# Performance work log

Hardware: AMD Instinct MI355X
Metric: run time of the kernel (lower is better)

## Reference

```python
import jax, jax.numpy as jnp
import numpy as np

N = 100000
E = 1600000
IN_C = 256
HID = 256
OUT_C = 10
G = 64  # number of graphs in batch


def setup_inputs() -> dict:
    key = jax.random.key(0)
    k1, k2, k3, k4, k5, k6, k7 = jax.random.split(key, 7)
    x = jax.random.normal(k1, (N, IN_C), dtype=jnp.float32)
    edge_index = jax.random.randint(k2, (2, E), 0, N, dtype=jnp.int64)
    batch = jnp.sort(jax.random.randint(k3, (N,), 0, G, dtype=jnp.int64))
    # GCNConv weight (glorot-ish) and bias
    W1 = jax.random.normal(k4, (IN_C, HID), dtype=jnp.float32) / np.sqrt(IN_C)
    b1 = jnp.zeros((HID,), dtype=jnp.float32)
    # final Linear
    W2 = jax.random.normal(k5, (HID, OUT_C), dtype=jnp.float32) / np.sqrt(HID)
    b2 = jax.random.normal(k6, (OUT_C,), dtype=jnp.float32) * 0.01
    return {"x": x, "edge_index": edge_index, "batch": batch,
            "W1": W1, "b1": b1, "W2": W2, "b2": b2}


def reference(x, edge_index, batch, W1, b1, W2, b2):
    # ---- GCNConv(in_channels, hidden_dim), add_self_loops=True, symmetric norm ----
    src = edge_index[0]
    dst = edge_index[1]
    loop = jnp.arange(N, dtype=src.dtype)
    src = jnp.concatenate([src, loop])  # [E+N]
    dst = jnp.concatenate([dst, loop])
    # degree on destination nodes (incl. self-loops) -> >= 1 everywhere
    deg = jax.ops.segment_sum(jnp.ones_like(dst, dtype=x.dtype), dst, num_segments=N)
    dinv = jax.lax.rsqrt(deg)  # deg >= 1, safe
    h = x @ W1  # linear transform first (PyG GCNConv order)
    norm = dinv[src] * dinv[dst]  # [E+N]
    msgs = h[src] * norm[:, None]  # gather + scale
    agg = jax.ops.segment_sum(msgs, dst, num_segments=N) + b1  # scatter-add + bias
    # ---- relu; dropout is identity in eval mode ----
    hrelu = jax.nn.relu(agg)
    # ---- global_mean_pool over batch ids ----
    sums = jax.ops.segment_sum(hrelu, batch, num_segments=G)
    counts = jax.ops.segment_sum(jnp.ones((N,), dtype=x.dtype), batch, num_segments=G)
    pooled = sums / jnp.maximum(counts, 1.0)[:, None]  # [G, HID]
    # ---- final linear ----
    return pooled @ W2 + b2
```

## Files before the change

kernel.cpp:

```cpp
#include <hip/hip_runtime.h>

#define NN 100000
#define EE 1600000
#define C 256
#define OUTC 10
#define NG 64

#define NBK 391
#define CHUNK 16384
#define NBLK1 ((EE + CHUNK - 1) / CHUNK)
#define PADSLACK 2048

#define NODES_PER_GROUP 8
#define NODES_PER_BLOCK 32

typedef __bf16 bf16x8 __attribute__((ext_vector_type(8)));
typedef float f32x4 __attribute__((ext_vector_type(4)));
typedef float f32x2 __attribute__((ext_vector_type(2)));

__device__ __forceinline__ ushort f2bf(float f) {
    unsigned u = __float_as_uint(f);
    return (ushort)((u + 0x7fffu + ((u >> 16) & 1u)) >> 16);
}
__device__ __forceinline__ bf16x8 as_bf16x8(uint4 v) {
    union { uint4 u; bf16x8 b; } c; c.u = v; return c.b;
}

__device__ __forceinline__ uchar f2fp8(float f) {
    return (uchar)(__builtin_amdgcn_cvt_pk_fp8_f32(f, 0.f, 0, false) & 0xff);
}
__device__ __forceinline__ void acc_fp8x4(float4& s, unsigned v) {
    f32x2 lo = __builtin_amdgcn_cvt_pk_f32_fp8(v, false);
    f32x2 hi = __builtin_amdgcn_cvt_pk_f32_fp8(v, true);
    s.x += lo[0]; s.y += lo[1]; s.z += hi[0]; s.w += hi[1];
}

__global__ __launch_bounds__(1024) void count_kernel(const int* __restrict__ batch,
                                                     float* __restrict__ cnt) {
    __shared__ int h[NG];
    if (threadIdx.x < NG) h[threadIdx.x] = 0;
    __syncthreads();
    int i = blockIdx.x * blockDim.x + threadIdx.x;
    if (i < NN) atomicAdd(&h[batch[i]], 1);
    __syncthreads();
    if (threadIdx.x < NG) {
        int v = h[threadIdx.x];
        if (v > 0) atomicAdd(&cnt[threadIdx.x], (float)v);
    }
}

__global__ __launch_bounds__(256) void bucket_hist_kernel(const int* __restrict__ ei,
                                                          int* __restrict__ bhist) {
    __shared__ int h[NBK];
    for (int t = threadIdx.x; t < NBK; t += 256) h[t] = 0;
    __syncthreads();
    const int base = blockIdx.x * CHUNK;
    const int end = min(base + CHUNK, EE);
    for (int e = base + threadIdx.x; e < end; e += 256)
        atomicAdd(&h[ei[EE + e] >> 8], 1);
    __syncthreads();
    for (int t = threadIdx.x; t < NBK; t += 256)
        if (h[t]) atomicAdd(&bhist[t], h[t]);
}

__global__ __launch_bounds__(512) void bucket_scan_kernel(const int* __restrict__ bhist,
                                                          int* __restrict__ bbase,
                                                          int* __restrict__ bcur) {
    __shared__ int sc[512];
    const int t = threadIdx.x;
    int v = (t < NBK) ? bhist[t] : 0;
    sc[t] = v;
    __syncthreads();
    for (int off = 1; off < 512; off <<= 1) {
        int tmp = (t >= off) ? sc[t - off] : 0;
        __syncthreads();
        sc[t] += tmp;
        __syncthreads();
    }
    int excl = sc[t] - v;
    if (t < NBK) { bbase[t] = excl; bcur[t] = excl; }
    if (t == 0) bbase[NBK] = sc[511];
}

__global__ __launch_bounds__(256) void bucket_scatter_kernel(const int* __restrict__ ei,
                                                             int* __restrict__ bcur,
                                                             unsigned* __restrict__ bmaj) {
    __shared__ int h[NBK];
    for (int t = threadIdx.x; t < NBK; t += 256) h[t] = 0;
    __syncthreads();
    const int base = blockIdx.x * CHUNK;
    const int end = min(base + CHUNK, EE);
    for (int e = base + threadIdx.x; e < end; e += 256)
        atomicAdd(&h[ei[EE + e] >> 8], 1);
    __syncthreads();
    for (int t = threadIdx.x; t < NBK; t += 256) {
        int c = h[t];
        h[t] = c ? atomicAdd(&bcur[t], c) : 0;
    }
    __syncthreads();
    for (int e = base + threadIdx.x; e < end; e += 256) {
        int d = ei[EE + e];
        int s = ei[e];
        int b = d >> 8;
        int p = atomicAdd(&h[b], 1);
        bmaj[p] = (unsigned)s | ((unsigned)(d & 255) << 17);
    }
}

__global__ __launch_bounds__(256) void bucket_csr_kernel(const unsigned* __restrict__ bmaj,
                                                         const int* __restrict__ bbase,
                                                         int* __restrict__ rowend,
                                                         float* __restrict__ dinv,
                                                         int* __restrict__ csrcol) {
    __shared__ int h[256];
    __shared__ int sc[256];
    __shared__ int cur[256];
    const int b = blockIdx.x;
    const int t = threadIdx.x;
    const int e0 = bbase[b], e1 = bbase[b + 1];
    const int region0 = e0 + b * PADSLACK;
    h[t] = 0;
    __syncthreads();
    for (int e = e0 + t; e < e1; e += 256)
        atomicAdd(&h[bmaj[e] >> 17], 1);
    __syncthreads();
    int deg = h[t];
    int pd = (deg + 7) & ~7;
    sc[t] = pd;
    __syncthreads();
    for (int off = 1; off < 256; off <<= 1) {
        int tmp = (t >= off) ? sc[t - off] : 0;
        __syncthreads();
        sc[t] += tmp;
        __syncthreads();
    }
    int pstart = region0 + sc[t] - pd;
    int node = b * 256 + t;
    if (node < NN) {
        rowend[node] = pstart + pd;
        dinv[node] = rsqrtf((float)deg + 1.0f);
        for (int j = deg; j < pd; j++) csrcol[pstart + j] = NN;
    }
    cur[t] = pstart;
    __syncthreads();
    for (int e = e0 + t; e < e1; e += 256) {
        unsigned v = bmaj[e];
        int p = atomicAdd(&cur[v >> 17], 1);
        csrcol[p] = (int)(v & 0x1FFFFu);
    }
}

__global__ __launch_bounds__(256) void w1pack_kernel(const float* __restrict__ W1,
                                                     ushort* __restrict__ w1f,
                                                     unsigned* __restrict__ gz) {
    int t = blockIdx.x * 256 + threadIdx.x;
    if (blockIdx.x == 0 && threadIdx.x < 64) gz[threadIdx.x] = 0;
    int k = t >> 8, n = t & 255;
    int kb = k >> 5, q = (k >> 3) & 3, j = k & 7;
    int nt = n >> 4, ln = (n & 15) + q * 16;
    w1f[(size_t)(((kb * 16 + nt) * 64) + ln) * 8 + j] = f2bf(W1[t]);
}

__global__ __launch_bounds__(256) void gemm_mfma_kernel(const float* __restrict__ x,
                                                        const ushort* __restrict__ w1f,
                                                        const float* __restrict__ dinv,
                                                        uchar* __restrict__ g) {
    const int lane = threadIdx.x & 63;
    const int wid = threadIdx.x >> 6;
    const int wave = blockIdx.x * 4 + wid;
    const int r0 = wave * 32;
    if (r0 >= NN) return;
    const int mrow = lane & 15;
    const int q = lane >> 4;

    f32x4 acc[2][16];
    #pragma unroll
    for (int mt = 0; mt < 2; mt++)
        #pragma unroll
        for (int nt = 0; nt < 16; nt++)
            acc[mt][nt] = (f32x4){0.f, 0.f, 0.f, 0.f};

    const float* xp0 = x + (size_t)(r0 + mrow) * C + q * 8;
    const float* xp1 = xp0 + (size_t)16 * C;
    const ushort* bp = w1f + (size_t)lane * 8;

    #pragma unroll 1
    for (int kb = 0; kb < 8; kb++) {
        const int ko = kb * 32;
        float4 a0lo = *(const float4*)(xp0 + ko);
        float4 a0hi = *(const float4*)(xp0 + ko + 4);
        float4 a1lo = *(const float4*)(xp1 + ko);
        float4 a1hi = *(const float4*)(xp1 + ko + 4);
        bf16x8 a0, a1;
        a0[0] = (__bf16)a0lo.x; a0[1] = (__bf16)a0lo.y;
        a0[2] = (__bf16)a0lo.z; a0[3] = (__bf16)a0lo.w;
        a0[4] = (__bf16)a0hi.x; a0[5] = (__bf16)a0hi.y;
        a0[6] = (__bf16)a0hi.z; a0[7] = (__bf16)a0hi.w;
        a1[0] = (__bf16)a1lo.x; a1[1] = (__bf16)a1lo.y;
        a1[2] = (__bf16)a1lo.z; a1[3] = (__bf16)a1lo.w;
        a1[4] = (__bf16)a1hi.x; a1[5] = (__bf16)a1hi.y;
        a1[6] = (__bf16)a1hi.z; a1[7] = (__bf16)a1hi.w;

        const ushort* bkb = bp + (size_t)kb * 16 * 512;
        #pragma unroll
        for (int nt = 0; nt < 16; nt++) {
            bf16x8 bb = as_bf16x8(*(const uint4*)(bkb + (size_t)nt * 512));
            acc[0][nt] = __builtin_amdgcn_mfma_f32_16x16x32_bf16(a0, bb, acc[0][nt], 0, 0, 0);
            acc[1][nt] = __builtin_amdgcn_mfma_f32_16x16x32_bf16(a1, bb, acc[1][nt], 0, 0, 0);
        }
    }

    #pragma unroll
    for (int mt = 0; mt < 2; mt++) {
        #pragma unroll
        for (int r = 0; r < 4; r++) {
            int row = r0 + mt * 16 + q * 4 + r;
            float dv = dinv[row];
            uchar* gp = g + (size_t)row * C + mrow;
            #pragma unroll
            for (int nt = 0; nt < 16; nt++)
                gp[nt * 16] = f2fp8(acc[mt][nt][r] * dv);
        }
    }
}

__global__ __launch_bounds__(256) void agg_pool_kernel(const unsigned* __restrict__ g32,
                                                       const int* __restrict__ rowend,
                                                       const int* __restrict__ csrcol,
                                                       const int* __restrict__ bbase,
                                                       const float* __restrict__ dinv,
                                                       const float* __restrict__ b1,
                                                       const int* __restrict__ batch,
                                                       float* __restrict__ sums) {
    const int lane = threadIdx.x & 63;
    const int wid = threadIdx.x >> 6;
    const int c4 = lane * 4;
    const int nodeA = blockIdx.x * NODES_PER_BLOCK + wid * NODES_PER_GROUP;
    const float4 bv = *(const float4*)&b1[c4];

    int rprev;
    if ((nodeA & 255) == 0) {
        int b = nodeA >> 8;
        rprev = bbase[b] + b * PADSLACK;
    } else {
        rprev = rowend[nodeA - 1];
    }

    float4 pool = make_float4(0.f, 0.f, 0.f, 0.f);
    int curb = -1;
    #pragma unroll 1
    for (int i = nodeA; i < nodeA + NODES_PER_GROUP; i++) {
        int r1 = rowend[i];
        int r0 = rprev;
        rprev = r1;
        int bi = batch[i];
        if (bi != curb) {
            if (curb >= 0) {
                atomicAdd(&sums[curb * C + c4 + 0], pool.x);
                atomicAdd(&sums[curb * C + c4 + 1], pool.y);
                atomicAdd(&sums[curb * C + c4 + 2], pool.z);
                atomicAdd(&sums[curb * C + c4 + 3], pool.w);
            }
            curb = bi;
            pool = make_float4(0.f, 0.f, 0.f, 0.f);
        }
        float4 s = make_float4(0.f, 0.f, 0.f, 0.f);
        acc_fp8x4(s, g32[(size_t)i * 64 + lane]);
        #pragma unroll 1
        for (int e = r0; e < r1; e += 8) {
            int i0 = csrcol[e],     i1 = csrcol[e + 1];
            int i2 = csrcol[e + 2], i3 = csrcol[e + 3];
            int i4 = csrcol[e + 4], i5 = csrcol[e + 5];
            int i6 = csrcol[e + 6], i7 = csrcol[e + 7];
            unsigned v0 = g32[(size_t)i0 * 64 + lane];
            unsigned v1 = g32[(size_t)i1 * 64 + lane];
            unsigned v2 = g32[(size_t)i2 * 64 + lane];
            unsigned v3 = g32[(size_t)i3 * 64 + lane];
            unsigned v4 = g32[(size_t)i4 * 64 + lane];
            unsigned v5 = g32[(size_t)i5 * 64 + lane];
            unsigned v6 = g32[(size_t)i6 * 64 + lane];
            unsigned v7 = g32[(size_t)i7 * 64 + lane];
            acc_fp8x4(s, v0); acc_fp8x4(s, v1); acc_fp8x4(s, v2); acc_fp8x4(s, v3);
            acc_fp8x4(s, v4); acc_fp8x4(s, v5); acc_fp8x4(s, v6); acc_fp8x4(s, v7);
        }
        float dv = dinv[i];
        pool.x += fmaxf(fmaf(dv, s.x, bv.x), 0.f);
        pool.y += fmaxf(fmaf(dv, s.y, bv.y), 0.f);
        pool.z += fmaxf(fmaf(dv, s.z, bv.z), 0.f);
        pool.w += fmaxf(fmaf(dv, s.w, bv.w), 0.f);
    }
    if (curb >= 0) {
        atomicAdd(&sums[curb * C + c4 + 0], pool.x);
        atomicAdd(&sums[curb * C + c4 + 1], pool.y);
        atomicAdd(&sums[curb * C + c4 + 2], pool.z);
        atomicAdd(&sums[curb * C + c4 + 3], pool.w);
    }
}

__global__ __launch_bounds__(256) void final_kernel(const float* __restrict__ sums,
                                                    const float* __restrict__ cnt,
                                                    const float* __restrict__ W2,
                                                    const float* __restrict__ b2,
                                                    float* __restrict__ out) {
    __shared__ float p[C];
    int gi = blockIdx.x;
    float cdiv = fmaxf(cnt[gi], 1.0f);
    p[threadIdx.x] = sums[gi * C + threadIdx.x] / cdiv;
    __syncthreads();
    if (threadIdx.x < OUTC) {
        float acc = b2[threadIdx.x];
        for (int k = 0; k < C; k++) acc += p[k] * W2[k * OUTC + threadIdx.x];
        out[gi * OUTC + threadIdx.x] = acc;
    }
}

extern "C" void kernel_launch(void* const* d_in, const int* in_sizes, int n_in,
                              void* d_out, int out_size, void* d_ws, size_t ws_size,
                              hipStream_t stream) {
    const float* x     = (const float*)d_in[0];
    const int*   ei    = (const int*)d_in[1];
    const int*   batch = (const int*)d_in[2];
    const float* W1    = (const float*)d_in[3];
    const float* b1    = (const float*)d_in[4];
    const float* W2    = (const float*)d_in[5];
    const float* b2    = (const float*)d_in[6];
    float* out = (float*)d_out;

    char* w = (char*)d_ws;
    size_t off = 0;
    auto carve = [&](size_t bytes) {
        void* p = w + off;
        off = (off + bytes + 255) & ~(size_t)255;
        return p;
    };
    uchar*    g        = (uchar*)   carve((size_t)(NN + 1) * C);
    int*      rowend   = (int*)     carve((size_t)NN * 4);
    float*    dinv     = (float*)   carve((size_t)NN * 4);
    int*      csrcol   = (int*)     carve((size_t)(EE + NBK * PADSLACK) * 4);
    unsigned* bmaj     = (unsigned*)carve((size_t)EE * 4);
    int*      bbase    = (int*)     carve((size_t)(NBK + 1) * 4);
    int*      bcur     = (int*)     carve((size_t)NBK * 4);
    ushort*   w1f      = (ushort*)  carve((size_t)C * C * 2);
    int*      bhist    = (int*)     carve((size_t)NBK * 4);
    float*    sums     = (float*)   carve((size_t)NG * C * 4);
    float*    cnt      = (float*)   carve((size_t)NG * 4);
    size_t zero_bytes = (size_t)((char*)cnt + (size_t)NG * 4 - (char*)bhist);

    hipMemsetAsync(bhist, 0, zero_bytes, stream);

    bucket_hist_kernel<<<NBLK1, 256, 0, stream>>>(ei, bhist);
    bucket_scan_kernel<<<1, 512, 0, stream>>>(bhist, bbase, bcur);
    bucket_scatter_kernel<<<NBLK1, 256, 0, stream>>>(ei, bcur, bmaj);
    bucket_csr_kernel<<<NBK, 256, 0, stream>>>(bmaj, bbase, rowend, dinv, csrcol);
    count_kernel<<<(NN + 1023) / 1024, 1024, 0, stream>>>(batch, cnt);
    w1pack_kernel<<<C * C / 256, 256, 0, stream>>>(W1, w1f, (unsigned*)(g + (size_t)NN * C));
    gemm_mfma_kernel<<<(NN / 32 + 3) / 4, 256, 0, stream>>>(x, w1f, dinv, g);
    agg_pool_kernel<<<NN / NODES_PER_BLOCK, 256, 0, stream>>>(
        (const unsigned*)g, rowend, csrcol, bbase, dinv, b1, batch, sums);
    final_kernel<<<NG, 256, 0, stream>>>(sums, cnt, W2, b2, out);
}
```

Before: 425.7 us.

## Split aggregation into four column-slice passes with lane-group edge parallelism

```diff
diff --git a/kernel.cpp b/kernel.cpp
--- a/kernel.cpp
+++ b/kernel.cpp
@@ -7,12 +7,13 @@
 #define NG 64
 
 #define NBK 391
-#define CHUNK 16384
+#define CHUNK 2048
 #define NBLK1 ((EE + CHUNK - 1) / CHUNK)
 #define PADSLACK 2048
 
 #define NODES_PER_GROUP 8
 #define NODES_PER_BLOCK 32
+#define NPASS 4
 
 typedef __bf16 bf16x8 __attribute__((ext_vector_type(8)));
 typedef float f32x4 __attribute__((ext_vector_type(4)));
@@ -118,7 +119,7 @@
     const int b = blockIdx.x;
     const int t = threadIdx.x;
     const int e0 = bbase[b], e1 = bbase[b + 1];
-    const int region0 = e0 + b * PADSLACK;
+    const int region0 = ((e0 + 7) & ~7) + b * PADSLACK;
     h[t] = 0;
     __syncthreads();
     for (int e = e0 + t; e < e1; e += 256)
@@ -231,17 +232,21 @@
                                                        const float* __restrict__ dinv,
                                                        const float* __restrict__ b1,
                                                        const int* __restrict__ batch,
-                                                       float* __restrict__ sums) {
+                                                       float* __restrict__ sums,
+                                                       const int pass) {
     const int lane = threadIdx.x & 63;
     const int wid = threadIdx.x >> 6;
-    const int c4 = lane * 4;
+    const int gq = lane >> 4;
+    const int cl = lane & 15;
+    const int cbase = pass * 64 + cl * 4;
     const int nodeA = blockIdx.x * NODES_PER_BLOCK + wid * NODES_PER_GROUP;
-    const float4 bv = *(const float4*)&b1[c4];
+    const float4 bv = *(const float4*)&b1[cbase];
+    const unsigned* gslice = g32 + (size_t)pass * 16 + cl;
 
     int rprev;
     if ((nodeA & 255) == 0) {
         int b = nodeA >> 8;
-        rprev = bbase[b] + b * PADSLACK;
+        rprev = ((bbase[b] + 7) & ~7) + b * PADSLACK;
     } else {
         rprev = rowend[nodeA - 1];
     }
@@ -255,45 +260,49 @@
         rprev = r1;
         int bi = batch[i];
         if (bi != curb) {
-            if (curb >= 0) {
-                atomicAdd(&sums[curb * C + c4 + 0], pool.x);
-                atomicAdd(&sums[curb * C + c4 + 1], pool.y);
-                atomicAdd(&sums[curb * C + c4 + 2], pool.z);
-                atomicAdd(&sums[curb * C + c4 + 3], pool.w);
+            if (curb >= 0 && gq == 0) {
+                atomicAdd(&sums[curb * C + cbase + 0], pool.x);
+                atomicAdd(&sums[curb * C + cbase + 1], pool.y);
+                atomicAdd(&sums[curb * C + cbase + 2], pool.z);
+                atomicAdd(&sums[curb * C + cbase + 3], pool.w);
             }
             curb = bi;
             pool = make_float4(0.f, 0.f, 0.f, 0.f);
         }
         float4 s = make_float4(0.f, 0.f, 0.f, 0.f);
-        acc_fp8x4(s, g32[(size_t)i * 64 + lane]);
+        if (gq == 0) acc_fp8x4(s, gslice[(size_t)i * 64]);
         #pragma unroll 1
         for (int e = r0; e < r1; e += 8) {
-            int i0 = csrcol[e],     i1 = csrcol[e + 1];
-            int i2 = csrcol[e + 2], i3 = csrcol[e + 3];
-            int i4 = csrcol[e + 4], i5 = csrcol[e + 5];
-            int i6 = csrcol[e + 6], i7 = csrcol[e + 7];
-            unsigned v0 = g32[(size_t)i0 * 64 + lane];
-            unsigned v1 = g32[(size_t)i1 * 64 + lane];
-            unsigned v2 = g32[(size_t)i2 * 64 + lane];
-            unsigned v3 = g32[(size_t)i3 * 64 + lane];
-            unsigned v4 = g32[(size_t)i4 * 64 + lane];
-            unsigned v5 = g32[(size_t)i5 * 64 + lane];
-            unsigned v6 = g32[(size_t)i6 * 64 + lane];
-            unsigned v7 = g32[(size_t)i7 * 64 + lane];
-            acc_fp8x4(s, v0); acc_fp8x4(s, v1); acc_fp8x4(s, v2); acc_fp8x4(s, v3);
-            acc_fp8x4(s, v4); acc_fp8x4(s, v5); acc_fp8x4(s, v6); acc_fp8x4(s, v7);
+            int4 iv0 = *(const int4*)(csrcol + e);
+            int4 iv1 = *(const int4*)(csrcol + e + 4);
+            int ia = iv0.x;
+            ia = (gq == 1) ? iv0.y : ia;
+            ia = (gq == 2) ? iv0.z : ia;
+            ia = (gq == 3) ? iv0.w : ia;
+            int ib = iv1.x;
+            ib = (gq == 1) ? iv1.y : ib;
+            ib = (gq == 2) ? iv1.z : ib;
+            ib = (gq == 3) ? iv1.w : ib;
+            unsigned va = gslice[(size_t)ia * 64];
+            unsigned vb = gslice[(size_t)ib * 64];
+            acc_fp8x4(s, va);
+            acc_fp8x4(s, vb);
         }
+        s.x += __shfl_xor(s.x, 16); s.y += __shfl_xor(s.y, 16);
+        s.z += __shfl_xor(s.z, 16); s.w += __shfl_xor(s.w, 16);
+        s.x += __shfl_xor(s.x, 32); s.y += __shfl_xor(s.y, 32);
+        s.z += __shfl_xor(s.z, 32); s.w += __shfl_xor(s.w, 32);
         float dv = dinv[i];
         pool.x += fmaxf(fmaf(dv, s.x, bv.x), 0.f);
         pool.y += fmaxf(fmaf(dv, s.y, bv.y), 0.f);
         pool.z += fmaxf(fmaf(dv, s.z, bv.z), 0.f);
         pool.w += fmaxf(fmaf(dv, s.w, bv.w), 0.f);
     }
-    if (curb >= 0) {
-        atomicAdd(&sums[curb * C + c4 + 0], pool.x);
-        atomicAdd(&sums[curb * C + c4 + 1], pool.y);
-        atomicAdd(&sums[curb * C + c4 + 2], pool.z);
-        atomicAdd(&sums[curb * C + c4 + 3], pool.w);
+    if (curb >= 0 && gq == 0) {
+        atomicAdd(&sums[curb * C + cbase + 0], pool.x);
+        atomicAdd(&sums[curb * C + cbase + 1], pool.y);
+        atomicAdd(&sums[curb * C + cbase + 2], pool.z);
+        atomicAdd(&sums[curb * C + cbase + 3], pool.w);
     }
 }
 
@@ -336,7 +345,7 @@
     uchar*    g        = (uchar*)   carve((size_t)(NN + 1) * C);
     int*      rowend   = (int*)     carve((size_t)NN * 4);
     float*    dinv     = (float*)   carve((size_t)NN * 4);
-    int*      csrcol   = (int*)     carve((size_t)(EE + NBK * PADSLACK) * 4);
+    int*      csrcol   = (int*)     carve((size_t)(EE + 8 + NBK * PADSLACK) * 4);
     unsigned* bmaj     = (unsigned*)carve((size_t)EE * 4);
     int*      bbase    = (int*)     carve((size_t)(NBK + 1) * 4);
     int*      bcur     = (int*)     carve((size_t)NBK * 4);
@@ -355,7 +364,8 @@
     count_kernel<<<(NN + 1023) / 1024, 1024, 0, stream>>>(batch, cnt);
     w1pack_kernel<<<C * C / 256, 256, 0, stream>>>(W1, w1f, (unsigned*)(g + (size_t)NN * C));
     gemm_mfma_kernel<<<(NN / 32 + 3) / 4, 256, 0, stream>>>(x, w1f, dinv, g);
-    agg_pool_kernel<<<NN / NODES_PER_BLOCK, 256, 0, stream>>>(
-        (const unsigned*)g, rowend, csrcol, bbase, dinv, b1, batch, sums);
+    for (int pass = 0; pass < NPASS; pass++)
+        agg_pool_kernel<<<NN / NODES_PER_BLOCK, 256, 0, stream>>>(
+            (const unsigned*)g, rowend, csrcol, bbase, dinv, b1, batch, sums, pass);
     final_kernel<<<NG, 256, 0, stream>>>(sums, cnt, W2, b2, out);
 }
```

After: 655.5 us. 1.54x slower.

## Double-buffer CSR gathers in aggregation with aligned vector index loads

Applied to the files above, without the earlier changes.

```diff
diff --git a/kernel.cpp b/kernel.cpp
--- a/kernel.cpp
+++ b/kernel.cpp
@@ -7,7 +7,7 @@
 #define NG 64
 
 #define NBK 391
-#define CHUNK 16384
+#define CHUNK 2048
 #define NBLK1 ((EE + CHUNK - 1) / CHUNK)
 #define PADSLACK 2048
 
@@ -118,7 +118,7 @@
     const int b = blockIdx.x;
     const int t = threadIdx.x;
     const int e0 = bbase[b], e1 = bbase[b + 1];
-    const int region0 = e0 + b * PADSLACK;
+    const int region0 = ((e0 + 7) & ~7) + b * PADSLACK;
     h[t] = 0;
     __syncthreads();
     for (int e = e0 + t; e < e1; e += 256)
@@ -224,24 +224,44 @@
     }
 }
 
-__global__ __launch_bounds__(256) void agg_pool_kernel(const unsigned* __restrict__ g32,
-                                                       const int* __restrict__ rowend,
-                                                       const int* __restrict__ csrcol,
-                                                       const int* __restrict__ bbase,
-                                                       const float* __restrict__ dinv,
-                                                       const float* __restrict__ b1,
-                                                       const int* __restrict__ batch,
-                                                       float* __restrict__ sums) {
+#define LOADB(p, E) do {                                                     \
+    int4 _i0 = *(const int4*)(csrcol + (E));                                 \
+    int4 _i1 = *(const int4*)(csrcol + (E) + 4);                             \
+    p##0 = gp[(size_t)_i0.x * 64];                                           \
+    p##1 = gp[(size_t)_i0.y * 64];                                           \
+    p##2 = gp[(size_t)_i0.z * 64];                                           \
+    p##3 = gp[(size_t)_i0.w * 64];                                           \
+    p##4 = gp[(size_t)_i1.x * 64];                                           \
+    p##5 = gp[(size_t)_i1.y * 64];                                           \
+    p##6 = gp[(size_t)_i1.z * 64];                                           \
+    p##7 = gp[(size_t)_i1.w * 64];                                           \
+} while (0)
+
+#define ACCB(p) do {                                                         \
+    acc_fp8x4(s, p##0); acc_fp8x4(s, p##1); acc_fp8x4(s, p##2);              \
+    acc_fp8x4(s, p##3); acc_fp8x4(s, p##4); acc_fp8x4(s, p##5);              \
+    acc_fp8x4(s, p##6); acc_fp8x4(s, p##7);                                  \
+} while (0)
+
+__global__ __launch_bounds__(256, 4) void agg_pool_kernel(const unsigned* __restrict__ g32,
+                                                          const int* __restrict__ rowend,
+                                                          const int* __restrict__ csrcol,
+                                                          const int* __restrict__ bbase,
+                                                          const float* __restrict__ dinv,
+                                                          const float* __restrict__ b1,
+                                                          const int* __restrict__ batch,
+                                                          float* __restrict__ sums) {
     const int lane = threadIdx.x & 63;
     const int wid = threadIdx.x >> 6;
     const int c4 = lane * 4;
     const int nodeA = blockIdx.x * NODES_PER_BLOCK + wid * NODES_PER_GROUP;
     const float4 bv = *(const float4*)&b1[c4];
+    const unsigned* gp = g32 + lane;
 
     int rprev;
     if ((nodeA & 255) == 0) {
         int b = nodeA >> 8;
-        rprev = bbase[b] + b * PADSLACK;
+        rprev = ((bbase[b] + 7) & ~7) + b * PADSLACK;
     } else {
         rprev = rowend[nodeA - 1];
     }
@@ -265,23 +285,30 @@
             pool = make_float4(0.f, 0.f, 0.f, 0.f);
         }
         float4 s = make_float4(0.f, 0.f, 0.f, 0.f);
-        acc_fp8x4(s, g32[(size_t)i * 64 + lane]);
-        #pragma unroll 1
-        for (int e = r0; e < r1; e += 8) {
-            int i0 = csrcol[e],     i1 = csrcol[e + 1];
-            int i2 = csrcol[e + 2], i3 = csrcol[e + 3];
-            int i4 = csrcol[e + 4], i5 = csrcol[e + 5];
-            int i6 = csrcol[e + 6], i7 = csrcol[e + 7];
-            unsigned v0 = g32[(size_t)i0 * 64 + lane];
-            unsigned v1 = g32[(size_t)i1 * 64 + lane];
-            unsigned v2 = g32[(size_t)i2 * 64 + lane];
-            unsigned v3 = g32[(size_t)i3 * 64 + lane];
-            unsigned v4 = g32[(size_t)i4 * 64 + lane];
-            unsigned v5 = g32[(size_t)i5 * 64 + lane];
-            unsigned v6 = g32[(size_t)i6 * 64 + lane];
-            unsigned v7 = g32[(size_t)i7 * 64 + lane];
-            acc_fp8x4(s, v0); acc_fp8x4(s, v1); acc_fp8x4(s, v2); acc_fp8x4(s, v3);
-            acc_fp8x4(s, v4); acc_fp8x4(s, v5); acc_fp8x4(s, v6); acc_fp8x4(s, v7);
+        unsigned vself = gp[(size_t)i * 64];
+        unsigned A0, A1, A2, A3, A4, A5, A6, A7;
+        unsigned B0, B1, B2, B3, B4, B5, B6, B7;
+        int e = r0;
+        if (e < r1) {
+            LOADB(A, e); e += 8;
+            if (e < r1) {
+                LOADB(B, e); e += 8;
+                acc_fp8x4(s, vself);
+                #pragma unroll 1
+                for (;;) {
+                    ACCB(A);
+                    if (e >= r1) { ACCB(B); break; }
+                    LOADB(A, e); e += 8;
+                    ACCB(B);
+                    if (e >= r1) { ACCB(A); break; }
+                    LOADB(B, e); e += 8;
+                }
+            } else {
+                acc_fp8x4(s, vself);
+                ACCB(A);
+            }
+        } else {
+            acc_fp8x4(s, vself);
         }
         float dv = dinv[i];
         pool.x += fmaxf(fmaf(dv, s.x, bv.x), 0.f);
@@ -336,7 +363,7 @@
     uchar*    g        = (uchar*)   carve((size_t)(NN + 1) * C);
     int*      rowend   = (int*)     carve((size_t)NN * 4);
     float*    dinv     = (float*)   carve((size_t)NN * 4);
-    int*      csrcol   = (int*)     carve((size_t)(EE + NBK * PADSLACK) * 4);
+    int*      csrcol   = (int*)     carve((size_t)(EE + 8 + NBK * PADSLACK) * 4);
     unsigned* bmaj     = (unsigned*)carve((size_t)EE * 4);
     int*      bbase    = (int*)     carve((size_t)(NBK + 1) * 4);
     int*      bcur     = (int*)     carve((size_t)NBK * 4);
```

New measurement: 424.6 us. No clear change (-0.3%).

## Software-pipeline CSR aggregation with inline-asm loads across node boundaries

Applied to the files above, without the earlier changes.

```diff
diff --git a/kernel.cpp b/kernel.cpp
--- a/kernel.cpp
+++ b/kernel.cpp
@@ -7,9 +7,9 @@
 #define NG 64
 
 #define NBK 391
-#define CHUNK 16384
+#define CHUNK 2048
 #define NBLK1 ((EE + CHUNK - 1) / CHUNK)
-#define PADSLACK 2048
+#define PADSLACK 2304
 
 #define NODES_PER_GROUP 8
 #define NODES_PER_BLOCK 32
@@ -17,6 +17,7 @@
 typedef __bf16 bf16x8 __attribute__((ext_vector_type(8)));
 typedef float f32x4 __attribute__((ext_vector_type(4)));
 typedef float f32x2 __attribute__((ext_vector_type(2)));
+typedef int   i32x4 __attribute__((ext_vector_type(4)));
 
 __device__ __forceinline__ ushort f2bf(float f) {
     unsigned u = __float_as_uint(f);
@@ -28,11 +29,6 @@
 
 __device__ __forceinline__ uchar f2fp8(float f) {
     return (uchar)(__builtin_amdgcn_cvt_pk_fp8_f32(f, 0.f, 0, false) & 0xff);
-}
-__device__ __forceinline__ void acc_fp8x4(float4& s, unsigned v) {
-    f32x2 lo = __builtin_amdgcn_cvt_pk_f32_fp8(v, false);
-    f32x2 hi = __builtin_amdgcn_cvt_pk_f32_fp8(v, true);
-    s.x += lo[0]; s.y += lo[1]; s.z += hi[0]; s.w += hi[1];
 }
 
 __global__ __launch_bounds__(1024) void count_kernel(const int* __restrict__ batch,
@@ -118,14 +114,15 @@
     const int b = blockIdx.x;
     const int t = threadIdx.x;
     const int e0 = bbase[b], e1 = bbase[b + 1];
-    const int region0 = e0 + b * PADSLACK;
+    const int region0 = ((e0 + 7) & ~7) + b * PADSLACK;
     h[t] = 0;
     __syncthreads();
     for (int e = e0 + t; e < e1; e += 256)
         atomicAdd(&h[bmaj[e] >> 17], 1);
     __syncthreads();
     int deg = h[t];
-    int pd = (deg + 7) & ~7;
+    int node = b * 256 + t;
+    int pd = (node < NN) ? ((deg + 8) & ~7) : 0;
     sc[t] = pd;
     __syncthreads();
     for (int off = 1; off < 256; off <<= 1) {
@@ -135,13 +132,13 @@
         __syncthreads();
     }
     int pstart = region0 + sc[t] - pd;
-    int node = b * 256 + t;
     if (node < NN) {
         rowend[node] = pstart + pd;
         dinv[node] = rsqrtf((float)deg + 1.0f);
-        for (int j = deg; j < pd; j++) csrcol[pstart + j] = NN;
-    }
-    cur[t] = pstart;
+        csrcol[pstart] = node;
+        for (int j = deg + 1; j < pd; j++) csrcol[pstart + j] = NN;
+    }
+    cur[t] = pstart + 1;
     __syncthreads();
     for (int e = e0 + t; e < e1; e += 256) {
         unsigned v = bmaj[e];
@@ -224,36 +221,148 @@
     }
 }
 
-__global__ __launch_bounds__(256) void agg_pool_kernel(const unsigned* __restrict__ g32,
-                                                       const int* __restrict__ rowend,
-                                                       const int* __restrict__ csrcol,
-                                                       const int* __restrict__ bbase,
-                                                       const float* __restrict__ dinv,
-                                                       const float* __restrict__ b1,
-                                                       const int* __restrict__ batch,
-                                                       float* __restrict__ sums) {
+
+#define GLOAD(dst, voff, base) \
+    asm volatile("global_load_dword %0, %1, %2" : "=v"(dst) : "v"(voff), "s"(base))
+#define GLOADX4(dst, voff, base) \
+    asm volatile("global_load_dwordx4 %0, %1, %2" : "=v"(dst) : "v"(voff), "s"(base))
+
+#define WAITI(N, Il, Ih) do {                                                  \
+    asm volatile("s_waitcnt vmcnt(" #N ")" : "+v"(Il), "+v"(Ih));              \
+    __builtin_amdgcn_sched_barrier(0);                                         \
+} while (0)
+
+#define WAITV(N, G, Il, Ih) do {                                               \
+    asm volatile("s_waitcnt vmcnt(" #N ")"                                     \
+        : "+v"(G##_0), "+v"(G##_1), "+v"(G##_2), "+v"(G##_3),                  \
+          "+v"(G##_4), "+v"(G##_5), "+v"(G##_6), "+v"(G##_7),                  \
+          "+v"(Il), "+v"(Ih));                                                 \
+    __builtin_amdgcn_sched_barrier(0);                                         \
+} while (0)
+
+#define ISSUE_G(G, Il, Ih) do {                                                \
+    unsigned _o0 = min((unsigned)Il[0], (unsigned)NN) * 256u + lane4;          \
+    unsigned _o1 = min((unsigned)Il[1], (unsigned)NN) * 256u + lane4;          \
+    unsigned _o2 = min((unsigned)Il[2], (unsigned)NN) * 256u + lane4;          \
+    unsigned _o3 = min((unsigned)Il[3], (unsigned)NN) * 256u + lane4;          \
+    unsigned _o4 = min((unsigned)Ih[0], (unsigned)NN) * 256u + lane4;          \
+    unsigned _o5 = min((unsigned)Ih[1], (unsigned)NN) * 256u + lane4;          \
+    unsigned _o6 = min((unsigned)Ih[2], (unsigned)NN) * 256u + lane4;          \
+    unsigned _o7 = min((unsigned)Ih[3], (unsigned)NN) * 256u + lane4;          \
+    GLOAD(G##_0, _o0, gb); GLOAD(G##_1, _o1, gb);                              \
+    GLOAD(G##_2, _o2, gb); GLOAD(G##_3, _o3, gb);                              \
+    GLOAD(G##_4, _o4, gb); GLOAD(G##_5, _o5, gb);                              \
+    GLOAD(G##_6, _o6, gb); GLOAD(G##_7, _o7, gb);                              \
+} while (0)
+
+#define ACC2(v) do {                                                           \
+    f32x2 _lo = __builtin_amdgcn_cvt_pk_f32_fp8((v), false);                   \
+    f32x2 _hi = __builtin_amdgcn_cvt_pk_f32_fp8((v), true);                    \
+    sA += _lo; sB += _hi;                                                      \
+} while (0)
+
+#define CONSUME(G) do {                                                        \
+    if (ec == curend) {                   \
+        *(float4*)&sstash[wid][nodem][lane][0] =                               \
+            make_float4(sA[0], sA[1], sB[0], sB[1]);                           \
+        sA = (f32x2){0.f, 0.f}; sB = (f32x2){0.f, 0.f};                        \
+        nodem++;                                                               \
+        curend = restash[wid][nodem];                                          \
+    }                                                                          \
+    ACC2(G##_0); ACC2(G##_1); ACC2(G##_2); ACC2(G##_3);                        \
+    ACC2(G##_4); ACC2(G##_5); ACC2(G##_6); ACC2(G##_7);                        \
+    ec += 8;                                                                   \
+} while (0)
+
+#define SUBITER(GX, GZ, IZl, IZh, IYl, IYh, cond) do {                         \
+    WAITV(10, GX, IZl, IZh);                                                   \
+    ISSUE_G(GZ, IZl, IZh);                                                     \
+    GLOADX4(IYl, voffI, csr4); GLOADX4(IYh, voffI + 16u, csr4);                \
+    voffI += 32u;                                                              \
+    if (cond) { CONSUME(GX); }                                                 \
+} while (0)
+
+__global__ __launch_bounds__(256, 4) void agg_pool_kernel(const unsigned* __restrict__ g32,
+                                                          const int* __restrict__ rowend,
+                                                          const int* __restrict__ csrcol,
+                                                          const int* __restrict__ bbase,
+                                                          const float* __restrict__ dinv,
+                                                          const float* __restrict__ b1,
+                                                          const int* __restrict__ batch,
+                                                          float* __restrict__ sums) {
+    __shared__ float sstash[4][NODES_PER_GROUP][64][4];
+    __shared__ int restash[4][NODES_PER_GROUP];
+
     const int lane = threadIdx.x & 63;
     const int wid = threadIdx.x >> 6;
+    const unsigned lane4 = (unsigned)lane * 4u;
     const int c4 = lane * 4;
     const int nodeA = blockIdx.x * NODES_PER_BLOCK + wid * NODES_PER_GROUP;
-    const float4 bv = *(const float4*)&b1[c4];
-
-    int rprev;
+    const unsigned* gb = g32;
+    const int* csr4 = csrcol;
+
+    int s0;
     if ((nodeA & 255) == 0) {
         int b = nodeA >> 8;
-        rprev = bbase[b] + b * PADSLACK;
+        s0 = ((bbase[b] + 7) & ~7) + b * PADSLACK;
     } else {
-        rprev = rowend[nodeA - 1];
-    }
-
+        s0 = rowend[nodeA - 1];
+    }
+    int4 reA = *(const int4*)(rowend + nodeA);
+    int4 reB = *(const int4*)(rowend + nodeA + 4);
+    if (lane == 0) {
+        restash[wid][0] = reA.x; restash[wid][1] = reA.y;
+        restash[wid][2] = reA.z; restash[wid][3] = reA.w;
+        restash[wid][4] = reB.x; restash[wid][5] = reB.y;
+        restash[wid][6] = reB.z; restash[wid][7] = reB.w;
+    }
+    const int B = (reB.w - s0) >> 3;
+    const int T = ((B + 2) / 3) * 3;
+
+    int ec = s0;
+    int curend = reA.x;
+    int nodem = 0;
+    f32x2 sA = (f32x2){0.f, 0.f}, sB = (f32x2){0.f, 0.f};
+
+    unsigned Ga_0, Ga_1, Ga_2, Ga_3, Ga_4, Ga_5, Ga_6, Ga_7;
+    unsigned Gb_0, Gb_1, Gb_2, Gb_3, Gb_4, Gb_5, Gb_6, Gb_7;
+    unsigned Gc_0, Gc_1, Gc_2, Gc_3, Gc_4, Gc_5, Gc_6, Gc_7;
+    i32x4 IaL, IaH, IbL, IbH, IcL, IcH;
+
+    asm volatile("s_waitcnt vmcnt(0)");
+    __builtin_amdgcn_sched_barrier(0);
+
+    unsigned voffI = (unsigned)s0 * 4u;
+    GLOADX4(IaL, voffI, csr4); GLOADX4(IaH, voffI + 16u, csr4); voffI += 32u;
+    GLOADX4(IbL, voffI, csr4); GLOADX4(IbH, voffI + 16u, csr4); voffI += 32u;
+    WAITI(2, IaL, IaH);
+    ISSUE_G(Ga, IaL, IaH);
+    GLOADX4(IcL, voffI, csr4); GLOADX4(IcH, voffI + 16u, csr4); voffI += 32u;
+    WAITI(10, IbL, IbH);
+    ISSUE_G(Gb, IbL, IbH);
+    GLOADX4(IaL, voffI, csr4); GLOADX4(IaH, voffI + 16u, csr4); voffI += 32u;
+
+    #pragma unroll 1
+    for (int k = 0; k < T; k += 3) {
+        SUBITER(Ga, Gc, IcL, IcH, IbL, IbH, (k < B));
+        SUBITER(Gb, Ga, IaL, IaH, IcL, IcH, (k + 1 < B));
+        SUBITER(Gc, Gb, IbL, IbH, IaL, IaH, (k + 2 < B));
+    }
+
+    asm volatile("s_waitcnt vmcnt(0)");
+    __builtin_amdgcn_sched_barrier(0);
+    *(float4*)&sstash[wid][NODES_PER_GROUP - 1][lane][0] =
+        make_float4(sA[0], sA[1], sB[0], sB[1]);
+
+    const float4 bv = *(const float4*)&b1[c4];
     float4 pool = make_float4(0.f, 0.f, 0.f, 0.f);
     int curb = -1;
     #pragma unroll 1
-    for (int i = nodeA; i < nodeA + NODES_PER_GROUP; i++) {
-        int r1 = rowend[i];
-        int r0 = rprev;
-        rprev = r1;
+    for (int n = 0; n < NODES_PER_GROUP; n++) {
+        int i = nodeA + n;
+        float4 sv = *(float4*)&sstash[wid][n][lane][0];
         int bi = batch[i];
+        float dv = dinv[i];
         if (bi != curb) {
             if (curb >= 0) {
                 atomicAdd(&sums[curb * C + c4 + 0], pool.x);
@@ -264,30 +373,10 @@
             curb = bi;
             pool = make_float4(0.f, 0.f, 0.f, 0.f);
         }
-        float4 s = make_float4(0.f, 0.f, 0.f, 0.f);
-        acc_fp8x4(s, g32[(size_t)i * 64 + lane]);
-        #pragma unroll 1
-        for (int e = r0; e < r1; e += 8) {
-            int i0 = csrcol[e],     i1 = csrcol[e + 1];
-            int i2 = csrcol[e + 2], i3 = csrcol[e + 3];
-            int i4 = csrcol[e + 4], i5 = csrcol[e + 5];
-            int i6 = csrcol[e + 6], i7 = csrcol[e + 7];
-            unsigned v0 = g32[(size_t)i0 * 64 + lane];
-            unsigned v1 = g32[(size_t)i1 * 64 + lane];
-            unsigned v2 = g32[(size_t)i2 * 64 + lane];
-            unsigned v3 = g32[(size_t)i3 * 64 + lane];
-            unsigned v4 = g32[(size_t)i4 * 64 + lane];
-            unsigned v5 = g32[(size_t)i5 * 64 + lane];
-            unsigned v6 = g32[(size_t)i6 * 64 + lane];
-            unsigned v7 = g32[(size_t)i7 * 64 + lane];
-            acc_fp8x4(s, v0); acc_fp8x4(s, v1); acc_fp8x4(s, v2); acc_fp8x4(s, v3);
-            acc_fp8x4(s, v4); acc_fp8x4(s, v5); acc_fp8x4(s, v6); acc_fp8x4(s, v7);
-        }
-        float dv = dinv[i];
-        pool.x += fmaxf(fmaf(dv, s.x, bv.x), 0.f);
-        pool.y += fmaxf(fmaf(dv, s.y, bv.y), 0.f);
-        pool.z += fmaxf(fmaf(dv, s.z, bv.z), 0.f);
-        pool.w += fmaxf(fmaf(dv, s.w, bv.w), 0.f);
+        pool.x += fmaxf(fmaf(dv, sv.x, bv.x), 0.f);
+        pool.y += fmaxf(fmaf(dv, sv.y, bv.y), 0.f);
+        pool.z += fmaxf(fmaf(dv, sv.z, bv.z), 0.f);
+        pool.w += fmaxf(fmaf(dv, sv.w, bv.w), 0.f);
     }
     if (curb >= 0) {
         atomicAdd(&sums[curb * C + c4 + 0], pool.x);
@@ -336,7 +425,7 @@
     uchar*    g        = (uchar*)   carve((size_t)(NN + 1) * C);
     int*      rowend   = (int*)     carve((size_t)NN * 4);
     float*    dinv     = (float*)   carve((size_t)NN * 4);
-    int*      csrcol   = (int*)     carve((size_t)(EE + NBK * PADSLACK) * 4);
+    int*      csrcol   = (int*)     carve((size_t)(EE + (size_t)NBK * PADSLACK + 128) * 4);
     unsigned* bmaj     = (unsigned*)carve((size_t)EE * 4);
     int*      bbase    = (int*)     carve((size_t)(NBK + 1) * 4);
     int*      bcur     = (int*)     carve((size_t)NBK * 4);
```

Measured after the change: 457.9 us. +7.6%, slower.
